# Performance work log

Hardware: AMD Instinct MI355X
Metric: run time of the kernel (lower is better)

The kernel has to match this reference:

```python
import jax, jax.numpy as jnp
import numpy as np

B, T, C, H = 8, 2048, 1024, 16
D = C // H  # head dim


def setup_inputs() -> dict:
    key = jax.random.key(0)
    k1, k2, k3 = jax.random.split(key, 3)
    x = jax.random.normal(k1, (B, T, C), dtype=jnp.float32)
    attention_mask = jnp.ones((B, 1, T), dtype=jnp.int32)
    w_attn = jax.random.normal(k2, (C, 3 * C), dtype=jnp.float32) * 0.02
    b_attn = jnp.zeros((3 * C,), dtype=jnp.float32)
    w_proj = jax.random.normal(k3, (C, C), dtype=jnp.float32) * (0.02 / np.sqrt(2 * 12))
    b_proj = jnp.zeros((C,), dtype=jnp.float32)
    return {"x": x, "attention_mask": attention_mask, "w_attn": w_attn,
            "b_attn": b_attn, "w_proj": w_proj, "b_proj": b_proj}


def reference(x, attention_mask, w_attn, b_attn, w_proj, b_proj):
    Bx, Tx, Cx = x.shape
    qkv = x @ w_attn + b_attn                      # [B,T,3C]
    q, k, v = jnp.split(qkv, 3, axis=2)
    def heads(t):
        return t.reshape(Bx, Tx, H, D).transpose(0, 2, 1, 3)  # [B,H,T,D]
    q, k, v = heads(q), heads(k), heads(v)
    phi_q = jax.nn.elu(q) + 1.0
    phi_k = jax.nn.elu(k) + 1.0
    valid_keys = jnp.any(attention_mask > 0, axis=1).astype(x.dtype)  # [B,T]
    mask = valid_keys[:, None, :, None]            # [B,1,T,1]
    phi_k = phi_k * mask
    v = v * mask
    kv = jnp.einsum('bhtd,bhtf->bhdf', phi_k, v)   # [B,H,D,D]
    k_sum = jnp.sum(phi_k, axis=2, keepdims=True)  # [B,H,1,D]
    numerator = jnp.einsum('bhtd,bhdf->bhtf', phi_q, kv)       # [B,H,T,D]
    denominator = jnp.einsum('bhtd,bhrd->bhtr', phi_q, k_sum)  # [B,H,T,1]
    denominator = jnp.maximum(denominator, 1e-08)
    y = numerator / denominator
    y = y.transpose(0, 2, 1, 3).reshape(Bx, Tx, Cx)
    return y @ w_proj + b_proj
```

## Files before the change

### kernel.cpp

```cpp
#include <hip/hip_runtime.h>

#define Tdim 2048

typedef __attribute__((ext_vector_type(8))) short bf16x8;
typedef __attribute__((ext_vector_type(4))) float f32x4;
typedef __attribute__((ext_vector_type(4))) short short4v;

#define GLOBAL_U32(p) ((const __attribute__((address_space(1))) unsigned int*)(p))
#define LDS_U32(p)    ((__attribute__((address_space(3))) unsigned int*)(p))

#define BARRIER() do { asm volatile("" ::: "memory"); \
                       __builtin_amdgcn_s_barrier(); \
                       asm volatile("" ::: "memory"); } while (0)

__device__ __forceinline__ float phi_f(float x) {
    return x > 0.f ? (x + 1.f) : __expf(x);
}
__device__ __forceinline__ short f2bf(float f) {
    unsigned u = __float_as_uint(f);
    u += 0x7fffu + ((u >> 16) & 1u);
    return (short)(u >> 16);
}
__device__ __forceinline__ float bf2f(short h) {
    return __uint_as_float(((unsigned)(unsigned short)h) << 16);
}


__global__ __launch_bounds__(256) void split_tile_kernel(
    const float* __restrict__ X, short* __restrict__ Hi, short* __restrict__ Lo)
{
    const int rt = blockIdx.x;
    const int cb = blockIdx.y;
    const int t = threadIdx.x;
    const int rl = t >> 4;
    const int cc = t & 15;

    const float* xp = X + ((size_t)rt * 16 + rl) * 1024 + cb * 128 + cc * 8;
    const float4 a = *(const float4*)xp;
    const float4 b = *(const float4*)(xp + 4);
    float v[8] = {a.x, a.y, a.z, a.w, b.x, b.y, b.z, b.w};
    bf16x8 h, l;
#pragma unroll
    for (int j = 0; j < 8; ++j) {
        const short hh = f2bf(v[j]);
        h[j] = hh;
        l[j] = f2bf(v[j] - bf2f(hh));
    }
    const int kt = cb * 4 + (cc >> 2);
    const int slot = ((cc & 3) << 4) | rl;
    const size_t off = ((size_t)rt * 32 + kt) * 512 + slot * 8;
    *(bf16x8*)(Hi + off) = h;
    *(bf16x8*)(Lo + off) = l;
}

__global__ __launch_bounds__(256) void w_tile_kernel(
    const float* __restrict__ W, int N,
    short* __restrict__ Thi, short* __restrict__ Tlo)
{
    const int tile = blockIdx.x * 4 + (threadIdx.x >> 6);
    const int nt = tile >> 5;
    const int kt = tile & 31;
    const int lane = threadIdx.x & 63;
    const int n = nt * 16 + (lane & 15);
    const int k = kt * 32 + (lane >> 4) * 8;
    const float* wp = W + (size_t)k * N + n;
    bf16x8 h, l;
#pragma unroll
    for (int j = 0; j < 8; ++j) {
        const float v = wp[(size_t)j * N];
        const short hh = f2bf(v);
        h[j] = hh;
        l[j] = f2bf(v - bf2f(hh));
    }
    const size_t off = (size_t)tile * 512 + lane * 8;
    *(bf16x8*)(Thi + off) = h;
    *(bf16x8*)(Tlo + off) = l;
}

template<int AMODE>
__global__ __launch_bounds__(512, 2) void gemm3_kernel(
    const short* __restrict__ Ahi, const short* __restrict__ Alo, int lda,
    const short* __restrict__ BThi, const short* __restrict__ BTlo,
    const float* __restrict__ bias, float* __restrict__ C,
    int K, int ldc)
{
    __shared__ short smem[65536];
    const int tid = threadIdx.x;
    const int lane = tid & 63;
    const int wid = tid >> 6;
    const int bx = blockIdx.x, by = blockIdx.y;
    const int wm = wid >> 2, wn = wid & 3;

    const size_t tilestep = (size_t)(K >> 5) * 512;

    const int sel = wid >> 1, half = wid & 1;
    const bool is_a_wave = (wid < 4);
    const short* gptr;
    if (sel >= 2) {
        const short* gb = (sel == 2) ? BThi : BTlo;
        gptr = gb + (size_t)(bx * 16 + half * 8) * tilestep + lane * 8;
    } else if (AMODE == 0) {
        const short* gb = (sel == 0) ? Ahi : Alo;
        gptr = gb + (size_t)(by * 16 + half * 8) * tilestep + lane * 8;
    } else {
        gptr = Ahi + (size_t)((by * 16 + half * 8) * 16) * 6144 + 2048 + lane * 8;
    }
    short* lw = smem + sel * 8192 + half * 4096;

    f32x4 acc[8][4];
#pragma unroll
    for (int i = 0; i < 8; ++i)
#pragma unroll
        for (int j = 0; j < 4; ++j) acc[i][j] = (f32x4){0.f, 0.f, 0.f, 0.f};

    auto stage = [&](int buf, int k0) {
        short* lb = lw + buf * 32768;
        if (AMODE == 0 || sel >= 2) {
            const short* g = gptr + (size_t)(k0 >> 5) * 512;
#pragma unroll
            for (int c = 0; c < 8; ++c)
                __builtin_amdgcn_global_load_lds(
                    GLOBAL_U32(g + (size_t)c * tilestep),
                    LDS_U32(lb + c * 512), 16, 0, 0);
        } else {
            const size_t koff = (size_t)(k0 >> 6) * 6144
                              + (size_t)((((k0 >> 5) & 1) << 1) | sel) * 512;
            const short* g = gptr + koff;
#pragma unroll
            for (int c = 0; c < 8; ++c)
                __builtin_amdgcn_global_load_lds(
                    GLOBAL_U32(g + (size_t)(c * 16) * 6144),
                    LDS_U32(lb + c * 512), 16, 0, 0);
        }
    };

    stage(0, 0);
    __syncthreads();

    const int fo = lane * 8;
    int cur = 0;
    for (int k0 = 0; k0 < K; k0 += 32) {
        const short* bp = smem + cur * 32768;
        const int k0n = (k0 + 32 < K) ? (k0 + 32) : 0;

        if (!is_a_wave) stage(cur ^ 1, k0n);
        bf16x8 bh[4], bl[4];
#pragma unroll
        for (int j = 0; j < 4; ++j) {
            bh[j] = *(const bf16x8*)(bp + 16384 + (wn * 4 + j) * 512 + fo);
            bl[j] = *(const bf16x8*)(bp + 24576 + (wn * 4 + j) * 512 + fo);
        }
        if (is_a_wave) asm volatile("s_waitcnt vmcnt(0)" ::: "memory");
        BARRIER();

        if (is_a_wave) stage(cur ^ 1, k0n);
        __builtin_amdgcn_s_setprio(1);
#pragma unroll
        for (int i = 0; i < 8; ++i) {
            const bf16x8 ah = *(const bf16x8*)(bp + (wm * 8 + i) * 512 + fo);
            const bf16x8 al = *(const bf16x8*)(bp + 8192 + (wm * 8 + i) * 512 + fo);
#pragma unroll
            for (int j = 0; j < 4; ++j) {
                acc[i][j] = __builtin_amdgcn_mfma_f32_16x16x32_bf16(ah, bh[j], acc[i][j], 0, 0, 0);
                acc[i][j] = __builtin_amdgcn_mfma_f32_16x16x32_bf16(al, bh[j], acc[i][j], 0, 0, 0);
                acc[i][j] = __builtin_amdgcn_mfma_f32_16x16x32_bf16(ah, bl[j], acc[i][j], 0, 0, 0);
            }
        }
        __builtin_amdgcn_s_setprio(0);
        if (!is_a_wave) asm volatile("s_waitcnt vmcnt(0)" ::: "memory");
        BARRIER();
        cur ^= 1;
    }

    const int fr = lane & 15, fq = lane >> 4;
#pragma unroll
    for (int i = 0; i < 8; ++i) {
        const size_t row0 = (size_t)by * 256 + wm * 128 + i * 16 + fq * 4;
#pragma unroll
        for (int j = 0; j < 4; ++j) {
            const int col = bx * 256 + wn * 64 + j * 16 + fr;
            const float bv = bias[col];
            float* cp = C + row0 * (size_t)ldc + col;
#pragma unroll
            for (int r = 0; r < 4; ++r)
                cp[(size_t)r * ldc] = acc[i][j][r] + bv;
        }
    }
}

__global__ __launch_bounds__(256) void kv_part_kernel(
    const float* __restrict__ qkv, const int* __restrict__ attn,
    float* __restrict__ kvpart, float* __restrict__ kspart)
{
    __shared__ float ks[32][64];
    __shared__ float vs[32][64];

    const int chunk = blockIdx.x;
    const int bh = blockIdx.y;
    const int b = bh >> 4;
    const int h = bh & 15;
    const int tid = threadIdx.x;
    const int tx = tid & 15;
    const int ty = tid >> 4;
    const int l_t = tid >> 4;
    const int l_d = (tid & 15) << 2;

    const float* kb = qkv + (size_t)b * Tdim * 3072 + 1024 + h * 64;
    const float* vb = qkv + (size_t)b * Tdim * 3072 + 2048 + h * 64;
    const int* am = attn + b * Tdim;

    float acc[4][4];
#pragma unroll
    for (int i = 0; i < 4; ++i)
#pragma unroll
        for (int j = 0; j < 4; ++j) acc[i][j] = 0.f;
    float ksl = 0.f;

    for (int t0 = chunk * 256; t0 < (chunk + 1) * 256; t0 += 32) {
        __syncthreads();
#pragma unroll
        for (int rr = 0; rr < 2; ++rr) {
            const int t = l_t + rr * 16;
            const int gt = t0 + t;
            const float m = (am[gt] > 0) ? 1.f : 0.f;
            const float4 k4 = *(const float4*)(kb + (size_t)gt * 3072 + l_d);
            const float4 v4 = *(const float4*)(vb + (size_t)gt * 3072 + l_d);
            float4 kp, vp;
            kp.x = phi_f(k4.x) * m; kp.y = phi_f(k4.y) * m;
            kp.z = phi_f(k4.z) * m; kp.w = phi_f(k4.w) * m;
            vp.x = v4.x * m; vp.y = v4.y * m; vp.z = v4.z * m; vp.w = v4.w * m;
            *(float4*)&ks[t][l_d] = kp;
            *(float4*)&vs[t][l_d] = vp;
        }
        __syncthreads();
#pragma unroll
        for (int t = 0; t < 32; ++t) {
            float kr[4], vr[4];
            *(float4*)kr = *(const float4*)&ks[t][ty * 4];
            *(float4*)vr = *(const float4*)&vs[t][tx * 4];
#pragma unroll
            for (int i = 0; i < 4; ++i)
#pragma unroll
                for (int j = 0; j < 4; ++j)
                    acc[i][j] = fmaf(kr[i], vr[j], acc[i][j]);
        }
        if (tid < 64) {
#pragma unroll
            for (int t = 0; t < 32; ++t) ksl += ks[t][tid];
        }
    }

    float* ko = kvpart + ((size_t)bh * 8 + chunk) * 4096;
#pragma unroll
    for (int i = 0; i < 4; ++i) {
        float4 o;
        o.x = acc[i][0]; o.y = acc[i][1]; o.z = acc[i][2]; o.w = acc[i][3];
        *(float4*)(ko + (ty * 4 + i) * 64 + tx * 4) = o;
    }
    if (tid < 64) kspart[((size_t)bh * 8 + chunk) * 64 + tid] = ksl;
}

__global__ __launch_bounds__(256) void kv_reduce_kernel(
    const float* __restrict__ kvpart, const float* __restrict__ kspart,
    float* __restrict__ kv, float* __restrict__ ksum)
{
    const int bh = blockIdx.x;
    const int tid = threadIdx.x;
    const float4* p = (const float4*)(kvpart + (size_t)bh * 8 * 4096);
    float4 s0 = {0,0,0,0}, s1 = {0,0,0,0}, s2 = {0,0,0,0}, s3 = {0,0,0,0};
#pragma unroll
    for (int c = 0; c < 8; ++c) {
        const int base = c * 1024;
        float4 a = p[base + tid], b = p[base + 256 + tid],
               cc = p[base + 512 + tid], d = p[base + 768 + tid];
        s0.x += a.x; s0.y += a.y; s0.z += a.z; s0.w += a.w;
        s1.x += b.x; s1.y += b.y; s1.z += b.z; s1.w += b.w;
        s2.x += cc.x; s2.y += cc.y; s2.z += cc.z; s2.w += cc.w;
        s3.x += d.x; s3.y += d.y; s3.z += d.z; s3.w += d.w;
    }
    float4* o = (float4*)(kv + (size_t)bh * 4096);
    o[tid] = s0; o[256 + tid] = s1; o[512 + tid] = s2; o[768 + tid] = s3;
    if (tid < 64) {
        float ss = 0.f;
#pragma unroll
        for (int c = 0; c < 8; ++c) ss += kspart[((size_t)bh * 8 + c) * 64 + tid];
        ksum[bh * 64 + tid] = ss;
    }
}

__global__ __launch_bounds__(256) void attn_y_kernel(
    float* __restrict__ qkv, const float* __restrict__ kvin,
    const float* __restrict__ ksumin)
{
    __shared__ float qs[64][65];
    __shared__ float kvs[64][64];
    __shared__ float dinv[64];
    __shared__ float ksums[64];

    const int bh = blockIdx.y;
    const int b = bh >> 4;
    const int hh = bh & 15;
    const int t0 = blockIdx.x * 64;
    const int tid = threadIdx.x;
    const int tx = tid & 15;
    const int ty = tid >> 4;

    const float4* kvg = (const float4*)(kvin + (size_t)bh * 4096);
#pragma unroll
    for (int i = 0; i < 4; ++i)
        ((float4*)kvs)[tid + i * 256] = kvg[tid + i * 256];
    if (tid < 64) ksums[tid] = ksumin[bh * 64 + tid];

    float* qb = qkv + ((size_t)(b * Tdim + t0)) * 3072 + hh * 64;
#pragma unroll
    for (int rr = 0; rr < 4; ++rr) {
        const int t = (tid >> 4) + rr * 16;
        const int dd = (tid & 15) << 2;
        const float4 q4 = *(const float4*)(qb + (size_t)t * 3072 + dd);
        qs[t][dd + 0] = phi_f(q4.x);
        qs[t][dd + 1] = phi_f(q4.y);
        qs[t][dd + 2] = phi_f(q4.z);
        qs[t][dd + 3] = phi_f(q4.w);
    }
    __syncthreads();

    if (tid < 64) {
        float s = 0.f;
#pragma unroll
        for (int d = 0; d < 64; ++d) s = fmaf(qs[tid][d], ksums[d], s);
        dinv[tid] = 1.f / fmaxf(s, 1e-8f);
    }
    __syncthreads();

    float acc[4][4];
#pragma unroll
    for (int i = 0; i < 4; ++i)
#pragma unroll
        for (int j = 0; j < 4; ++j) acc[i][j] = 0.f;

#pragma unroll 4
    for (int d = 0; d < 64; ++d) {
        float qr[4];
        qr[0] = qs[ty * 4 + 0][d];
        qr[1] = qs[ty * 4 + 1][d];
        qr[2] = qs[ty * 4 + 2][d];
        qr[3] = qs[ty * 4 + 3][d];
        const float4 kr = *(const float4*)&kvs[d][tx * 4];
#pragma unroll
        for (int i = 0; i < 4; ++i) {
            acc[i][0] = fmaf(qr[i], kr.x, acc[i][0]);
            acc[i][1] = fmaf(qr[i], kr.y, acc[i][1]);
            acc[i][2] = fmaf(qr[i], kr.z, acc[i][2]);
            acc[i][3] = fmaf(qr[i], kr.w, acc[i][3]);
        }
    }

    short* yb = (short*)qkv;
    const int kl = tx >> 3;
    const int chunk = (tx & 7) >> 1;
    const int h4 = (tx & 1) * 4;
    const int gb2 = b * Tdim;
#pragma unroll
    for (int i = 0; i < 4; ++i) {
        const int t = ty * 4 + i;
        const int RT = ((gb2 + t0) >> 4) + (t >> 4);
        const float di = dinv[t];
        short4v hv, lv;
#pragma unroll
        for (int j = 0; j < 4; ++j) {
            const float val = acc[i][j] * di;
            const short h = f2bf(val);
            hv[j] = h;
            lv[j] = f2bf(val - bf2f(h));
        }
        const size_t tb = (size_t)(RT * 16 + hh) * 6144 + 2048
                        + (size_t)(kl * 2) * 512
                        + (((chunk << 4) | (t & 15)) * 8 + h4);
        *(short4v*)(yb + tb) = hv;
        *(short4v*)(yb + tb + 512) = lv;
    }
}

extern "C" void kernel_launch(void* const* d_in, const int* in_sizes, int n_in,
                              void* d_out, int out_size, void* d_ws, size_t ws_size,
                              hipStream_t stream)
{
    const float* x      = (const float*)d_in[0];
    const int*   attn   = (const int*)  d_in[1];
    const float* w_attn = (const float*)d_in[2];
    const float* b_attn = (const float*)d_in[3];
    const float* w_proj = (const float*)d_in[4];
    const float* b_proj = (const float*)d_in[5];
    float* out = (float*)d_out;

    char* ws = (char*)d_ws;
    size_t off = 0;
    auto alloc = [&](size_t bytes) { void* p = ws + off; off = (off + bytes + 255) & ~(size_t)255; return p; };
    float* qkv   = (float*)alloc((size_t)16384 * 3072 * 4);
    short* waThi = (short*)alloc((size_t)3072 * 1024 * 2);
    short* waTlo = (short*)alloc((size_t)3072 * 1024 * 2);
    short* wpThi = (short*)alloc((size_t)1024 * 1024 * 2);
    short* wpTlo = (short*)alloc((size_t)1024 * 1024 * 2);
    float* kvb   = (float*)alloc((size_t)128 * 4096 * 4);
    float* ksum  = (float*)alloc((size_t)128 * 64 * 4);

    short* xhi = (short*)d_out;
    short* xlo = xhi + (size_t)16384 * 1024;
    float* kvpart = (float*)d_out;
    float* kspart = (float*)((char*)d_out + (size_t)128 * 8 * 4096 * 4);

    split_tile_kernel<<<dim3(1024, 8), 256, 0, stream>>>(x, xhi, xlo);
    w_tile_kernel<<<1536, 256, 0, stream>>>(w_attn, 3072, waThi, waTlo);
    w_tile_kernel<<<512, 256, 0, stream>>>(w_proj, 1024, wpThi, wpTlo);
    gemm3_kernel<0><<<dim3(12, 64), 512, 0, stream>>>(xhi, xlo, 0, waThi, waTlo, b_attn, qkv, 1024, 3072);
    kv_part_kernel<<<dim3(8, 128), 256, 0, stream>>>(qkv, attn, kvpart, kspart);
    kv_reduce_kernel<<<128, 256, 0, stream>>>(kvpart, kspart, kvb, ksum);
    attn_y_kernel<<<dim3(32, 128), 256, 0, stream>>>(qkv, kvb, ksum);
    gemm3_kernel<2><<<dim3(4, 64), 512, 0, stream>>>((const short*)qkv, (const short*)qkv, 0,
                                                     wpThi, wpTlo, b_proj, out, 1024, 1024);
}
```

Before: 570.7 us.

## Compute phi(Q)·KV with split-bf16 MFMA and pre-tiled KV from reduce kernel

The reduce kernel now transposes the summed KV matrix through LDS and writes it as hi/lo bf16 pairs in an MFMA-ready tile layout. The attention-output kernel loads that layout directly into LDS with global_load_lds, builds phi(Q) hi/lo fragments in registers, computes the denominator with a shuffle reduction, and runs three bf16 16x16x32 MFMAs per tile instead of an FP32 FMA loop. The aim is to cut the scalar FMA work and the LDS staging of Q. In exchange the output is written as scalar 2-byte stores instead of short4 vectors, and the three-term bf16 split gives slightly lower accuracy than fp32.

```diff
diff --git a/kernel.cpp b/kernel.cpp
--- a/kernel.cpp
+++ b/kernel.cpp
@@ -262,8 +262,9 @@
 
 __global__ __launch_bounds__(256) void kv_reduce_kernel(
     const float* __restrict__ kvpart, const float* __restrict__ kspart,
-    float* __restrict__ kv, float* __restrict__ ksum)
-{
+    short* __restrict__ kvT, float* __restrict__ ksum)
+{
+    __shared__ float kvs[64][68];
     const int bh = blockIdx.x;
     const int tid = threadIdx.x;
     const float4* p = (const float4*)(kvpart + (size_t)bh * 8 * 4096);
@@ -278,8 +279,33 @@
         s2.x += cc.x; s2.y += cc.y; s2.z += cc.z; s2.w += cc.w;
         s3.x += d.x; s3.y += d.y; s3.z += d.z; s3.w += d.w;
     }
-    float4* o = (float4*)(kv + (size_t)bh * 4096);
-    o[tid] = s0; o[256 + tid] = s1; o[512 + tid] = s2; o[768 + tid] = s3;
+    const int d0 = tid >> 4, f0 = (tid & 15) * 4;
+    *(float4*)&kvs[d0 +  0][f0] = s0;
+    *(float4*)&kvs[d0 + 16][f0] = s1;
+    *(float4*)&kvs[d0 + 32][f0] = s2;
+    *(float4*)&kvs[d0 + 48][f0] = s3;
+    __syncthreads();
+
+    short* kvb = kvT + (size_t)bh * 8192;
+#pragma unroll
+    for (int pp = 0; pp < 2; ++pp) {
+        const int sid = tid * 2 + pp;
+        const int tt = sid >> 6;
+        const int L = sid & 63;
+        const int nt = tt >> 1, kt = tt & 1;
+        const int f = nt * 16 + (L & 15);
+        const int dd = kt * 32 + (L >> 4) * 8;
+        bf16x8 h, l;
+#pragma unroll
+        for (int e = 0; e < 8; ++e) {
+            const float v = kvs[dd + e][f];
+            const short hh = f2bf(v);
+            h[e] = hh;
+            l[e] = f2bf(v - bf2f(hh));
+        }
+        *(bf16x8*)(kvb + tt * 512 + L * 8) = h;
+        *(bf16x8*)(kvb + 4096 + tt * 512 + L * 8) = l;
+    }
     if (tid < 64) {
         float ss = 0.f;
 #pragma unroll
@@ -289,95 +315,97 @@
 }
 
 __global__ __launch_bounds__(256) void attn_y_kernel(
-    float* __restrict__ qkv, const float* __restrict__ kvin,
+    float* __restrict__ qkv, const short* __restrict__ kvT,
     const float* __restrict__ ksumin)
 {
-    __shared__ float qs[64][65];
-    __shared__ float kvs[64][64];
-    __shared__ float dinv[64];
-    __shared__ float ksums[64];
+    __shared__ short kvs[8192];
+    __shared__ float den_s[4][16];
 
     const int bh = blockIdx.y;
     const int b = bh >> 4;
     const int hh = bh & 15;
     const int t0 = blockIdx.x * 64;
     const int tid = threadIdx.x;
-    const int tx = tid & 15;
-    const int ty = tid >> 4;
-
-    const float4* kvg = (const float4*)(kvin + (size_t)bh * 4096);
-#pragma unroll
-    for (int i = 0; i < 4; ++i)
-        ((float4*)kvs)[tid + i * 256] = kvg[tid + i * 256];
-    if (tid < 64) ksums[tid] = ksumin[bh * 64 + tid];
-
-    float* qb = qkv + ((size_t)(b * Tdim + t0)) * 3072 + hh * 64;
-#pragma unroll
-    for (int rr = 0; rr < 4; ++rr) {
-        const int t = (tid >> 4) + rr * 16;
-        const int dd = (tid & 15) << 2;
-        const float4 q4 = *(const float4*)(qb + (size_t)t * 3072 + dd);
-        qs[t][dd + 0] = phi_f(q4.x);
-        qs[t][dd + 1] = phi_f(q4.y);
-        qs[t][dd + 2] = phi_f(q4.z);
-        qs[t][dd + 3] = phi_f(q4.w);
-    }
+    const int lane = tid & 63;
+    const int wid = tid >> 6;
+
+    {
+        const short* src = kvT + (size_t)bh * 8192 + (wid * 4) * 512 + lane * 8;
+        short* dst = kvs + (wid * 4) * 512;
+#pragma unroll
+        for (int t = 0; t < 4; ++t)
+            __builtin_amdgcn_global_load_lds(
+                GLOBAL_U32(src + t * 512), LDS_U32(dst + t * 512), 16, 0, 0);
+    }
+
+    const int grow = b * Tdim + t0 + wid * 16 + (lane & 15);
+    const int kc = (lane >> 4) * 8;
+    const float* qp = qkv + (size_t)grow * 3072 + hh * 64 + kc;
+    const float* kp = ksumin + bh * 64 + kc;
+    bf16x8 ah[2], al[2];
+    float den = 0.f;
+#pragma unroll
+    for (int ks = 0; ks < 2; ++ks) {
+        const float4 a = *(const float4*)(qp + ks * 32);
+        const float4 c = *(const float4*)(qp + ks * 32 + 4);
+        const float4 u = *(const float4*)(kp + ks * 32);
+        const float4 w = *(const float4*)(kp + ks * 32 + 4);
+        float qv[8] = {a.x, a.y, a.z, a.w, c.x, c.y, c.z, c.w};
+        float sv[8] = {u.x, u.y, u.z, u.w, w.x, w.y, w.z, w.w};
+#pragma unroll
+        for (int e = 0; e < 8; ++e) {
+            const float ph = phi_f(qv[e]);
+            den = fmaf(ph, sv[e], den);
+            const short hi = f2bf(ph);
+            ah[ks][e] = hi;
+            al[ks][e] = f2bf(ph - bf2f(hi));
+        }
+    }
+    den += __shfl_xor(den, 16);
+    den += __shfl_xor(den, 32);
+    if ((lane >> 4) == 0) den_s[wid][lane & 15] = den;
     __syncthreads();
 
-    if (tid < 64) {
-        float s = 0.f;
-#pragma unroll
-        for (int d = 0; d < 64; ++d) s = fmaf(qs[tid][d], ksums[d], s);
-        dinv[tid] = 1.f / fmaxf(s, 1e-8f);
-    }
-    __syncthreads();
-
-    float acc[4][4];
-#pragma unroll
-    for (int i = 0; i < 4; ++i)
-#pragma unroll
-        for (int j = 0; j < 4; ++j) acc[i][j] = 0.f;
-
-#pragma unroll 4
-    for (int d = 0; d < 64; ++d) {
-        float qr[4];
-        qr[0] = qs[ty * 4 + 0][d];
-        qr[1] = qs[ty * 4 + 1][d];
-        qr[2] = qs[ty * 4 + 2][d];
-        qr[3] = qs[ty * 4 + 3][d];
-        const float4 kr = *(const float4*)&kvs[d][tx * 4];
-#pragma unroll
-        for (int i = 0; i < 4; ++i) {
-            acc[i][0] = fmaf(qr[i], kr.x, acc[i][0]);
-            acc[i][1] = fmaf(qr[i], kr.y, acc[i][1]);
-            acc[i][2] = fmaf(qr[i], kr.z, acc[i][2]);
-            acc[i][3] = fmaf(qr[i], kr.w, acc[i][3]);
-        }
-    }
+    f32x4 acc[4];
+#pragma unroll
+    for (int j = 0; j < 4; ++j) acc[j] = (f32x4){0.f, 0.f, 0.f, 0.f};
+#pragma unroll
+    for (int j = 0; j < 4; ++j) {
+#pragma unroll
+        for (int ks = 0; ks < 2; ++ks) {
+            const short* tb = kvs + (j * 2 + ks) * 512 + lane * 8;
+            const bf16x8 bhf = *(const bf16x8*)tb;
+            const bf16x8 blf = *(const bf16x8*)(tb + 4096);
+            acc[j] = __builtin_amdgcn_mfma_f32_16x16x32_bf16(ah[ks], bhf, acc[j], 0, 0, 0);
+            acc[j] = __builtin_amdgcn_mfma_f32_16x16x32_bf16(al[ks], bhf, acc[j], 0, 0, 0);
+            acc[j] = __builtin_amdgcn_mfma_f32_16x16x32_bf16(ah[ks], blf, acc[j], 0, 0, 0);
+        }
+    }
+
+    float dinv[4];
+#pragma unroll
+    for (int r = 0; r < 4; ++r)
+        dinv[r] = 1.f / fmaxf(den_s[wid][(lane >> 4) * 4 + r], 1e-8f);
 
     short* yb = (short*)qkv;
-    const int kl = tx >> 3;
-    const int chunk = (tx & 7) >> 1;
-    const int h4 = (tx & 1) * 4;
-    const int gb2 = b * Tdim;
-#pragma unroll
-    for (int i = 0; i < 4; ++i) {
-        const int t = ty * 4 + i;
-        const int RT = ((gb2 + t0) >> 4) + (t >> 4);
-        const float di = dinv[t];
-        short4v hv, lv;
-#pragma unroll
-        for (int j = 0; j < 4; ++j) {
-            const float val = acc[i][j] * di;
+    const int RT = ((b * Tdim + t0) >> 4) + wid;
+    const size_t rowbase = (size_t)(RT * 16 + hh) * 6144 + 2048;
+#pragma unroll
+    for (int j = 0; j < 4; ++j) {
+        const int c = j * 16 + (lane & 15);
+        const int kl = c >> 5;
+        const int cc = (c & 31) >> 3;
+        const int wi = c & 7;
+        const size_t so = rowbase + (size_t)(kl * 2) * 512
+                        + (size_t)(cc << 4) * 8 + wi;
+#pragma unroll
+        for (int r = 0; r < 4; ++r) {
+            const int rloc = (lane >> 4) * 4 + r;
+            const float val = acc[j][r] * dinv[r];
             const short h = f2bf(val);
-            hv[j] = h;
-            lv[j] = f2bf(val - bf2f(h));
-        }
-        const size_t tb = (size_t)(RT * 16 + hh) * 6144 + 2048
-                        + (size_t)(kl * 2) * 512
-                        + (((chunk << 4) | (t & 15)) * 8 + h4);
-        *(short4v*)(yb + tb) = hv;
-        *(short4v*)(yb + tb + 512) = lv;
+            yb[so + (size_t)rloc * 8] = h;
+            yb[so + 512 + (size_t)rloc * 8] = f2bf(val - bf2f(h));
+        }
     }
 }
 
@@ -401,7 +429,7 @@
     short* waTlo = (short*)alloc((size_t)3072 * 1024 * 2);
     short* wpThi = (short*)alloc((size_t)1024 * 1024 * 2);
     short* wpTlo = (short*)alloc((size_t)1024 * 1024 * 2);
-    float* kvb   = (float*)alloc((size_t)128 * 4096 * 4);
+    short* kvbT  = (short*)alloc((size_t)128 * 8192 * 2);
     float* ksum  = (float*)alloc((size_t)128 * 64 * 4);
 
     short* xhi = (short*)d_out;
@@ -414,8 +442,8 @@
     w_tile_kernel<<<512, 256, 0, stream>>>(w_proj, 1024, wpThi, wpTlo);
     gemm3_kernel<0><<<dim3(12, 64), 512, 0, stream>>>(xhi, xlo, 0, waThi, waTlo, b_attn, qkv, 1024, 3072);
     kv_part_kernel<<<dim3(8, 128), 256, 0, stream>>>(qkv, attn, kvpart, kspart);
-    kv_reduce_kernel<<<128, 256, 0, stream>>>(kvpart, kspart, kvb, ksum);
-    attn_y_kernel<<<dim3(32, 128), 256, 0, stream>>>(qkv, kvb, ksum);
+    kv_reduce_kernel<<<128, 256, 0, stream>>>(kvpart, kspart, kvbT, ksum);
+    attn_y_kernel<<<dim3(32, 128), 256, 0, stream>>>(qkv, kvbT, ksum);
     gemm3_kernel<2><<<dim3(4, 64), 512, 0, stream>>>((const short*)qkv, (const short*)qkv, 0,
                                                      wpThi, wpTlo, b_proj, out, 1024, 1024);
 }
```

New measurement: 573.3 us. No clear change (+0.5%).
